# Performance work log

Measured on AMD Instinct MI355X. Metric: run time of the kernel, lower is better.

## Reference

```python
import jax, jax.numpy as jnp
import numpy as np

N, E, H, NF, EF = 50000, 1600000, 128, 8, 2


def setup_inputs() -> dict:
    key = jax.random.key(0)
    ks = jax.random.split(key, 24)
    rn = lambda k, shp, s=0.05: jax.random.normal(k, shp, jnp.float32) * s
    inp = {
        "x": jax.random.normal(ks[0], (N, NF), jnp.float32),
        "edge_index": jax.random.randint(ks[1], (2, E), 0, N),
        "edge_attr": jax.random.normal(ks[2], (E, EF), jnp.float32),
        "enc_W": rn(ks[3], (NF, H)),
        "enc_b": jnp.zeros((H,), jnp.float32),
        "bn_g": jnp.ones((H,), jnp.float32),
        "bn_b": jnp.zeros((H,), jnp.float32),
    }
    i = 4
    for l in (1, 2, 3):
        inp[f"W{l}"] = rn(ks[i], (H, H))
        inp[f"asrc{l}"] = rn(ks[i + 1], (H,))
        inp[f"adst{l}"] = rn(ks[i + 2], (H,))
        inp[f"We{l}"] = rn(ks[i + 3], (EF, H))
        inp[f"ae{l}"] = rn(ks[i + 4], (H,))
        inp[f"b{l}"] = jnp.zeros((H,), jnp.float32)
        i += 5
    return inp


def _gat(h, src, dst, ea, W, a_s, a_d, We, a_e, b, n):
    # PyG GATConv, heads=1, concat=True, negative_slope=0.2
    g = h @ W                                   # [N, H] transformed nodes
    a_src = g @ a_s                             # [N] per-source attention term
    a_dst = g @ a_d                             # [N] per-target attention term
    a_edge = (ea @ We) @ a_e                    # [E'] edge-conditioned term
    logit = jax.nn.leaky_relu(a_src[src] + a_dst[dst] + a_edge, negative_slope=0.2)
    # scatter-softmax over incoming edges of each destination node
    m = jax.ops.segment_max(logit, dst, num_segments=n)
    e = jnp.exp(logit - m[dst])
    s = jax.ops.segment_sum(e, dst, num_segments=n)
    alpha = e / (s[dst] + 1e-16)                # [E']
    out = jax.ops.segment_sum(g[src] * alpha[:, None], dst, num_segments=n)
    return out + b


def _forward(x, edge_index, edge_attr, enc_W, enc_b, bn_g, bn_b,
             W1, asrc1, adst1, We1, ae1, b1,
             W2, asrc2, adst2, We2, ae2, b2,
             W3, asrc3, adst3, We3, ae3, b3):
    n = x.shape[0]
    # PyG add_self_loops=True with fill_value='mean' for edge_attr
    loop = jnp.arange(n)
    src = jnp.concatenate([edge_index[0], loop])
    dst = jnp.concatenate([edge_index[1], loop])
    ea = jnp.concatenate([edge_attr, jnp.broadcast_to(edge_attr.mean(0), (n, edge_attr.shape[1]))], axis=0)
    # node encoder: Linear -> BatchNorm1d (eval: running_mean=0, running_var=1) -> ReLU (dropout off)
    inv = np.float32(1.0 / np.sqrt(1.0 + 1e-5))
    h0 = jax.nn.relu((x @ enc_W + enc_b) * (bn_g * inv) + bn_b)
    h1 = jax.nn.relu(_gat(h0, src, dst, ea, W1, asrc1, adst1, We1, ae1, b1, n))
    h2 = jax.nn.relu(_gat(h1, src, dst, ea, W2, asrc2, adst2, We2, ae2, b2, n))
    h3 = _gat(h2, src, dst, ea, W3, asrc3, adst3, We3, ae3, b3, n)
    return h3 + h0


def reference(x, edge_index, edge_attr, enc_W, enc_b, bn_g, bn_b,
              W1, asrc1, adst1, We1, ae1, b1,
              W2, asrc2, adst2, We2, ae2, b2,
              W3, asrc3, adst3, We3, ae3, b3):
    return _forward(x, edge_index, edge_attr, enc_W, enc_b, bn_g, bn_b,
                    W1, asrc1, adst1, We1, ae1, b1,
                    W2, asrc2, adst2, We2, ae2, b2,
                    W3, asrc3, adst3, We3, ae3, b3)
```

## Files before the change

### kernel.cpp

```cpp
#include <hip/hip_runtime.h>
#include <math.h>


#define H 128
#define NF 8
#define EPB 4096
#define GR 64

__device__ __forceinline__ float wred_sum(float x) {
#pragma unroll
    for (int m = 32; m >= 1; m >>= 1) x += __shfl_xor(x, m, 64);
    return x;
}
__device__ __forceinline__ float wred_max(float x) {
#pragma unroll
    for (int m = 32; m >= 1; m >>= 1) x = fmaxf(x, __shfl_xor(x, m, 64));
    return x;
}
__device__ __forceinline__ ushort f2bf(float f) {
    uint u = __float_as_uint(f);
    uint r = (u + 0x7FFFu + ((u >> 16) & 1u)) >> 16;
    return (ushort)r;
}


__global__ void k_count(const int* __restrict__ ei, const float* __restrict__ ea,
                        int E, int nblk, int nbuckets, int* __restrict__ bucketTotal,
                        int* __restrict__ blockBase, float2* __restrict__ pmean) {
    __shared__ int hist[256];
    __shared__ float sx[4], sy[4];
    int t = threadIdx.x;
    int blk = blockIdx.x;
    hist[t] = 0;
    __syncthreads();
    int base = blk * EPB;
    float px = 0.f, py = 0.f;
#pragma unroll
    for (int i = 0; i < 16; ++i) {
        int e = base + i * 256 + t;
        if (e < E) {
            int d = ei[E + e];
            atomicAdd(&hist[d >> 8], 1);
            const float2 z = *(const float2*)(ea + 2 * (size_t)e);
            px += z.x; py += z.y;
        }
    }
    px = wred_sum(px); py = wred_sum(py);
    if ((t & 63) == 0) { sx[t >> 6] = px; sy[t >> 6] = py; }
    __syncthreads();
    if (t == 0) {
        pmean[blk] = make_float2(sx[0] + sx[1] + sx[2] + sx[3],
                                 sy[0] + sy[1] + sy[2] + sy[3]);
    }
    if (t < nbuckets) {
        int c = hist[t];
        int old = (c > 0) ? atomicAdd(&bucketTotal[t], c) : 0;
        blockBase[t * nblk + blk] = old;
    }
}

__global__ void k_scan_park(const int* __restrict__ bucketTotal, int nbuckets,
                            int* __restrict__ bucketBase, int* __restrict__ rowptr,
                            int N, int E, const float2* __restrict__ pmean, int nblk,
                            float invE,
                            const float* __restrict__ We1, const float* __restrict__ ae1,
                            const float* __restrict__ We2, const float* __restrict__ ae2,
                            const float* __restrict__ We3, const float* __restrict__ ae3,
                            float* __restrict__ park) {
    __shared__ int tmp[256];
    __shared__ float2 sp[4];
    __shared__ float smean[2];
    int t = threadIdx.x;
    float ax = 0.f, ay = 0.f;
    for (int i = t; i < nblk; i += 256) {
        float2 z = pmean[i];
        ax += z.x; ay += z.y;
    }
    ax = wred_sum(ax); ay = wred_sum(ay);
    if ((t & 63) == 0) sp[t >> 6] = make_float2(ax, ay);
    int v = (t < nbuckets) ? bucketTotal[t] : 0;
    tmp[t] = v;
    __syncthreads();
    for (int off = 1; off < 256; off <<= 1) {
        int q = (t >= off) ? tmp[t - off] : 0;
        __syncthreads();
        tmp[t] += q;
        __syncthreads();
    }
    bucketBase[t] = tmp[t] - v;
    if (t == 0) {
        bucketBase[256] = tmp[255];
        rowptr[N] = E;
        smean[0] = (sp[0].x + sp[1].x + sp[2].x + sp[3].x) * invE;
        smean[1] = (sp[0].y + sp[1].y + sp[2].y + sp[3].y) * invE;
    }
    __syncthreads();
    if (t < 192) {
        int l = t >> 6, q = t & 63;
        const float* We = (l == 0) ? We1 : ((l == 1) ? We2 : We3);
        const float* ae = (l == 0) ? ae1 : ((l == 1) ? ae2 : ae3);
        float p0 = We[q] * ae[q] + We[q + 64] * ae[q + 64];
        float p1 = We[H + q] * ae[q] + We[H + q + 64] * ae[q + 64];
        p0 = wred_sum(p0);
        p1 = wred_sum(p1);
        if (q == 0) {
            park[l * 3 + 0] = p0;
            park[l * 3 + 1] = p1;
            park[l * 3 + 2] = smean[0] * p0 + smean[1] * p1;
        }
    }
}

__global__ void k_place(const int* __restrict__ ei, const float* __restrict__ ea,
                        int E, int nblk, int nbuckets,
                        const int* __restrict__ bucketBase, const int* __restrict__ blockBase,
                        uint2* __restrict__ temp) {
    __shared__ int cnt[256];
    __shared__ int sbase[256];
    int t = threadIdx.x;
    int blk = blockIdx.x;
    cnt[t] = 0;
    if (t < nbuckets) sbase[t] = bucketBase[t] + blockBase[t * nblk + blk];
    __syncthreads();
    int base = blk * EPB;
#pragma unroll
    for (int i = 0; i < 16; ++i) {
        int e = base + i * 256 + t;
        if (e < E) {
            int s = ei[e];
            int d = ei[E + e];
            int b = d >> 8;
            int r = atomicAdd(&cnt[b], 1);
            const float2 z = *(const float2*)(ea + 2 * (size_t)e);
            uint w0 = (uint)s | ((uint)(d & 255) << 16);
            uint w1 = (uint)f2bf(z.x) | ((uint)f2bf(z.y) << 16);
            temp[sbase[b] + r] = make_uint2(w0, w1);
        }
    }
}

__global__ void k_fine(const uint2* __restrict__ temp, const int* __restrict__ bucketBase,
                       const float* __restrict__ park, int N,
                       int4* __restrict__ erec, int* __restrict__ rowptr) {
    __shared__ int hist[256];
    __shared__ int tmp[256];
    __shared__ int fb[256];
    __shared__ int cur[256];
    int b = blockIdx.x;
    int t = threadIdx.x;
    const int lo = bucketBase[b], hi = bucketBase[b + 1];
    hist[t] = 0;
    __syncthreads();
    for (int e = lo + t; e < hi; e += 256) {
        atomicAdd(&hist[(temp[e].x >> 16) & 255], 1);
    }
    __syncthreads();
    int v = hist[t];
    tmp[t] = v;
    __syncthreads();
    for (int off = 1; off < 256; off <<= 1) {
        int q = (t >= off) ? tmp[t - off] : 0;
        __syncthreads();
        tmp[t] += q;
        __syncthreads();
    }
    fb[t] = tmp[t] - v;
    cur[t] = 0;
    int dst = b * 256 + t;
    if (dst < N) rowptr[dst] = lo + fb[t];
    __syncthreads();
    const float c00 = park[0], c01 = park[1];
    const float c10 = park[3], c11 = park[4];
    const float c20 = park[6], c21 = park[7];
    for (int e = lo + t; e < hi; e += 256) {
        uint2 w = temp[e];
        int src = (int)(w.x & 0xFFFFu);
        int j = (int)((w.x >> 16) & 255u);
        float ex = __uint_as_float(w.y << 16);
        float ey = __uint_as_float(w.y & 0xffff0000u);
        int r = atomicAdd(&cur[j], 1);
        float f0 = c00 * ex + c01 * ey;
        float f1 = c10 * ex + c11 * ey;
        float f2 = c20 * ex + c21 * ey;
        erec[lo + fb[j] + r] = make_int4(src, __float_as_int(f0),
                                         __float_as_int(f1), __float_as_int(f2));
    }
}

__global__ void k_encoder(const float* __restrict__ x, const float* __restrict__ encW,
                          const float* __restrict__ encb, const float* __restrict__ bng,
                          const float* __restrict__ bnb, float* __restrict__ h0, int N) {
    __shared__ float xs[8 * NF];
    int tid = threadIdx.x;
    int nb = blockIdx.x * 8;
    if (tid < 64) {
        size_t idx = (size_t)nb * NF + tid;
        xs[tid] = (idx < (size_t)N * NF) ? x[idx] : 0.f;
    }
    __syncthreads();
    int jt = tid & 31, i = tid >> 5;
    int node = nb + i;
    int j4 = jt * 4;
    float ax = 0.f, ay = 0.f, az = 0.f, aw = 0.f;
#pragma unroll
    for (int k = 0; k < NF; ++k) {
        float hx = xs[i * NF + k];
        const float4 w = *(const float4*)(encW + k * H + j4);
        ax = fmaf(hx, w.x, ax); ay = fmaf(hx, w.y, ay);
        az = fmaf(hx, w.z, az); aw = fmaf(hx, w.w, aw);
    }
    if (node < N) {
        const float inv = 0.9999950000374997f;
        const float4 eb = *(const float4*)(encb + j4);
        const float4 gg = *(const float4*)(bng + j4);
        const float4 bb = *(const float4*)(bnb + j4);
        float4 o;
        o.x = fmaxf(0.f, (ax + eb.x) * (gg.x * inv) + bb.x);
        o.y = fmaxf(0.f, (ay + eb.y) * (gg.y * inv) + bb.y);
        o.z = fmaxf(0.f, (az + eb.z) * (gg.z * inv) + bb.z);
        o.w = fmaxf(0.f, (aw + eb.w) * (gg.w * inv) + bb.w);
        *(float4*)(h0 + (size_t)node * H + j4) = o;
    }
}

__global__ void k_gemm(const float* __restrict__ h, const float* __restrict__ W,
                       const float* __restrict__ avs, const float* __restrict__ avd,
                       ushort* __restrict__ gb, float* __restrict__ a_src,
                       float* __restrict__ a_dst, int N) {
    __shared__ float hs[GR * H];
    int tid = threadIdx.x;
    int nb = blockIdx.x * GR;
#pragma unroll
    for (int it = 0; it < 8; ++it) {
        int fi = it * 256 + tid;
        int r = fi >> 5;
        int c4 = (fi & 31) * 4;
        int node = nb + r;
        float4 v = make_float4(0.f, 0.f, 0.f, 0.f);
        if (node < N) v = *(const float4*)(h + (size_t)node * H + c4);
        *(float4*)(hs + r * H + c4) = v;
    }
    __syncthreads();
    const int jt = tid & 31;
    const int ig = tid >> 5;
    const int j4 = jt * 4;
    const int r0 = ig * 8;

    float acc[8][4];
#pragma unroll
    for (int r = 0; r < 8; ++r)
#pragma unroll
        for (int c = 0; c < 4; ++c) acc[r][c] = 0.f;

    for (int k = 0; k < H; k += 4) {
        const float4 w0 = *(const float4*)(W + (k + 0) * H + j4);
        const float4 w1 = *(const float4*)(W + (k + 1) * H + j4);
        const float4 w2 = *(const float4*)(W + (k + 2) * H + j4);
        const float4 w3 = *(const float4*)(W + (k + 3) * H + j4);
#pragma unroll
        for (int r = 0; r < 8; ++r) {
            const float4 hv = *(const float4*)(hs + (r0 + r) * H + k);
            acc[r][0] = fmaf(hv.x, w0.x, acc[r][0]);
            acc[r][1] = fmaf(hv.x, w0.y, acc[r][1]);
            acc[r][2] = fmaf(hv.x, w0.z, acc[r][2]);
            acc[r][3] = fmaf(hv.x, w0.w, acc[r][3]);
            acc[r][0] = fmaf(hv.y, w1.x, acc[r][0]);
            acc[r][1] = fmaf(hv.y, w1.y, acc[r][1]);
            acc[r][2] = fmaf(hv.y, w1.z, acc[r][2]);
            acc[r][3] = fmaf(hv.y, w1.w, acc[r][3]);
            acc[r][0] = fmaf(hv.z, w2.x, acc[r][0]);
            acc[r][1] = fmaf(hv.z, w2.y, acc[r][1]);
            acc[r][2] = fmaf(hv.z, w2.z, acc[r][2]);
            acc[r][3] = fmaf(hv.z, w2.w, acc[r][3]);
            acc[r][0] = fmaf(hv.w, w3.x, acc[r][0]);
            acc[r][1] = fmaf(hv.w, w3.y, acc[r][1]);
            acc[r][2] = fmaf(hv.w, w3.z, acc[r][2]);
            acc[r][3] = fmaf(hv.w, w3.w, acc[r][3]);
        }
    }

    const float4 s4 = *(const float4*)(avs + j4);
    const float4 d4 = *(const float4*)(avd + j4);
#pragma unroll
    for (int r = 0; r < 8; ++r) {
        int node = nb + r0 + r;
        float ps = acc[r][0] * s4.x + acc[r][1] * s4.y + acc[r][2] * s4.z + acc[r][3] * s4.w;
        float pd = acc[r][0] * d4.x + acc[r][1] * d4.y + acc[r][2] * d4.z + acc[r][3] * d4.w;
#pragma unroll
        for (int mm = 16; mm >= 1; mm >>= 1) {
            ps += __shfl_xor(ps, mm, 64);
            pd += __shfl_xor(pd, mm, 64);
        }
        if (node < N) {
            ushort4 o;
            o.x = f2bf(acc[r][0]); o.y = f2bf(acc[r][1]);
            o.z = f2bf(acc[r][2]); o.w = f2bf(acc[r][3]);
            *(ushort4*)(gb + (size_t)node * H + j4) = o;
            if (jt == 0) {
                a_src[node] = ps;
                a_dst[node] = pd;
            }
        }
    }
}

template <int RELU, int ADDH0, int LAYER>
__global__ void k_agg(const ushort* __restrict__ gb, const float* __restrict__ a_src,
                      const float* __restrict__ a_dst, const int* __restrict__ rowptr,
                      const int4* __restrict__ erec, const float* __restrict__ park,
                      const float* __restrict__ bias, const float* __restrict__ h0,
                      float* __restrict__ out, int N) {
    int wv = threadIdx.x >> 6;
    int lane = threadIdx.x & 63;
    int v = blockIdx.x * 4 + wv;
    if (v >= N) return;

    const int grp = lane >> 4;
    const int sub = lane & 15;
    const int ch8 = sub * 8;

    const float sa = park[LAYER * 3 + 2];
    const float adv = a_dst[v];
    float lself = a_src[v] + adv + sa;
    lself = (lself > 0.f) ? lself : 0.2f * lself;

    float m = lself;
    float s = 1.f;
    float acc[8];
    {
        const uint4 q = *(const uint4*)(gb + (size_t)v * H + ch8);
        float sel = (grp == 0) ? 1.f : 0.f;
        acc[0] = sel * __uint_as_float(q.x << 16);
        acc[1] = sel * __uint_as_float(q.x & 0xffff0000u);
        acc[2] = sel * __uint_as_float(q.y << 16);
        acc[3] = sel * __uint_as_float(q.y & 0xffff0000u);
        acc[4] = sel * __uint_as_float(q.z << 16);
        acc[5] = sel * __uint_as_float(q.z & 0xffff0000u);
        acc[6] = sel * __uint_as_float(q.w << 16);
        acc[7] = sel * __uint_as_float(q.w & 0xffff0000u);
    }

    const int rs = rowptr[v];
    const int re = rowptr[v + 1];
    for (int p0 = rs; p0 < re; p0 += 64) {
        int e = p0 + lane;
        bool val = e < re;
        int4 rec = val ? erec[e] : make_int4(0, 0, 0, 0);
        int sv = rec.x;
        float lg;
        if (val) {
            float aef = __int_as_float(LAYER == 0 ? rec.y : (LAYER == 1 ? rec.z : rec.w));
            lg = a_src[sv] + adv + aef;
            lg = (lg > 0.f) ? lg : 0.2f * lg;
        } else {
            lg = -INFINITY;
        }
        float cm = wred_max(lg);
        float nm = fmaxf(m, cm);
        float f = __expf(m - nm);
        float w = val ? __expf(lg - nm) : 0.f;
        float ws = wred_sum(w);
        s = s * f + ws;
#pragma unroll
        for (int k = 0; k < 8; ++k) acc[k] *= f;
        m = nm;

        int cnt = re - p0;
        if (cnt > 64) cnt = 64;
        const int cm1 = cnt - 1;
        const int iters = (cnt + 7) >> 3;

        int jA = grp, jB = grp + 4;
        int jAc = (jA <= cm1) ? jA : cm1;
        int jBc = (jB <= cm1) ? jB : cm1;
        float wA = __shfl(w, jAc, 64); if (jA > cm1) wA = 0.f;
        float wB = __shfl(w, jBc, 64); if (jB > cm1) wB = 0.f;
        int sA = __shfl(sv, jAc, 64);
        int sB = __shfl(sv, jBc, 64);
        uint4 qA = *(const uint4*)(gb + (size_t)sA * H + ch8);
        uint4 qB = *(const uint4*)(gb + (size_t)sB * H + ch8);

        for (int i = 0; i < iters; ++i) {
            int jA1 = (i + 1) * 8 + grp, jB1 = jA1 + 4;
            int jA1c = (jA1 <= cm1) ? jA1 : cm1;
            int jB1c = (jB1 <= cm1) ? jB1 : cm1;
            float wA1 = __shfl(w, jA1c, 64); if (jA1 > cm1) wA1 = 0.f;
            float wB1 = __shfl(w, jB1c, 64); if (jB1 > cm1) wB1 = 0.f;
            int sA1 = __shfl(sv, jA1c, 64);
            int sB1 = __shfl(sv, jB1c, 64);
            uint4 qA1 = *(const uint4*)(gb + (size_t)sA1 * H + ch8);
            uint4 qB1 = *(const uint4*)(gb + (size_t)sB1 * H + ch8);

            acc[0] = fmaf(wA, __uint_as_float(qA.x << 16), acc[0]);
            acc[1] = fmaf(wA, __uint_as_float(qA.x & 0xffff0000u), acc[1]);
            acc[2] = fmaf(wA, __uint_as_float(qA.y << 16), acc[2]);
            acc[3] = fmaf(wA, __uint_as_float(qA.y & 0xffff0000u), acc[3]);
            acc[4] = fmaf(wA, __uint_as_float(qA.z << 16), acc[4]);
            acc[5] = fmaf(wA, __uint_as_float(qA.z & 0xffff0000u), acc[5]);
            acc[6] = fmaf(wA, __uint_as_float(qA.w << 16), acc[6]);
            acc[7] = fmaf(wA, __uint_as_float(qA.w & 0xffff0000u), acc[7]);
            acc[0] = fmaf(wB, __uint_as_float(qB.x << 16), acc[0]);
            acc[1] = fmaf(wB, __uint_as_float(qB.x & 0xffff0000u), acc[1]);
            acc[2] = fmaf(wB, __uint_as_float(qB.y << 16), acc[2]);
            acc[3] = fmaf(wB, __uint_as_float(qB.y & 0xffff0000u), acc[3]);
            acc[4] = fmaf(wB, __uint_as_float(qB.z << 16), acc[4]);
            acc[5] = fmaf(wB, __uint_as_float(qB.z & 0xffff0000u), acc[5]);
            acc[6] = fmaf(wB, __uint_as_float(qB.w << 16), acc[6]);
            acc[7] = fmaf(wB, __uint_as_float(qB.w & 0xffff0000u), acc[7]);

            wA = wA1; wB = wB1; qA = qA1; qB = qB1;
        }
    }

#pragma unroll
    for (int k = 0; k < 8; ++k) {
        acc[k] += __shfl_xor(acc[k], 16, 64);
        acc[k] += __shfl_xor(acc[k], 32, 64);
    }

    if (grp == 0) {
        const float is = 1.f / s;
        const float4 b0 = *(const float4*)(bias + ch8);
        const float4 b1 = *(const float4*)(bias + ch8 + 4);
        float o[8];
        o[0] = acc[0] * is + b0.x; o[1] = acc[1] * is + b0.y;
        o[2] = acc[2] * is + b0.z; o[3] = acc[3] * is + b0.w;
        o[4] = acc[4] * is + b1.x; o[5] = acc[5] * is + b1.y;
        o[6] = acc[6] * is + b1.z; o[7] = acc[7] * is + b1.w;
        if (ADDH0) {
            const float4 ha = *(const float4*)(h0 + (size_t)v * H + ch8);
            const float4 hb = *(const float4*)(h0 + (size_t)v * H + ch8 + 4);
            o[0] += ha.x; o[1] += ha.y; o[2] += ha.z; o[3] += ha.w;
            o[4] += hb.x; o[5] += hb.y; o[6] += hb.z; o[7] += hb.w;
        }
        if (RELU) {
#pragma unroll
            for (int k = 0; k < 8; ++k) o[k] = fmaxf(o[k], 0.f);
        }
        *(float4*)(out + (size_t)v * H + ch8) = make_float4(o[0], o[1], o[2], o[3]);
        *(float4*)(out + (size_t)v * H + ch8 + 4) = make_float4(o[4], o[5], o[6], o[7]);
    }
}


extern "C" void kernel_launch(void* const* d_in, const int* in_sizes, int n_in,
                              void* d_out, int out_size, void* d_ws, size_t ws_size,
                              hipStream_t stream) {
    const float* x    = (const float*)d_in[0];
    const int*   ei   = (const int*)d_in[1];
    const float* ea   = (const float*)d_in[2];
    const float* encW = (const float*)d_in[3];
    const float* encb = (const float*)d_in[4];
    const float* bng  = (const float*)d_in[5];
    const float* bnb  = (const float*)d_in[6];
    const float *W[3], *asrc[3], *adst[3], *We[3], *aev[3], *bias[3];
    for (int l = 0; l < 3; ++l) {
        W[l]    = (const float*)d_in[7 + l * 6 + 0];
        asrc[l] = (const float*)d_in[7 + l * 6 + 1];
        adst[l] = (const float*)d_in[7 + l * 6 + 2];
        We[l]   = (const float*)d_in[7 + l * 6 + 3];
        aev[l]  = (const float*)d_in[7 + l * 6 + 4];
        bias[l] = (const float*)d_in[7 + l * 6 + 5];
    }
    const int N = in_sizes[0] / NF;
    const int E = in_sizes[1] / 2;
    float* out = (float*)d_out;

    const int NBu  = (N + 255) >> 8;
    const int nblk = (E + EPB - 1) / EPB;

    char* wp = (char*)d_ws;
    auto alloc = [&](size_t bytes) -> char* {
        char* p = wp;
        wp += (bytes + 255) & ~(size_t)255;
        return p;
    };
    float*  h0       = (float*)alloc((size_t)N * H * 4);
    float*  hA       = (float*)alloc((size_t)N * H * 4);
    ushort* gb       = (ushort*)alloc((size_t)N * H * 2);
    float*  a_src    = (float*)alloc((size_t)N * 4);
    float*  a_dst    = (float*)alloc((size_t)N * 4);
    int*    rowptr   = (int*)alloc((size_t)(N + 1) * 4);
    float*  park     = (float*)alloc(64);
    int*    bucketTotal = (int*)alloc(256 * 4);
    int*    bucketBase  = (int*)alloc(257 * 4);
    int*    blockBase   = (int*)alloc((size_t)NBu * nblk * 4);
    int4*   erec     = (int4*)alloc((size_t)E * 16);
    float2* pmean    = (float2*)alloc((size_t)nblk * 8);
    uint2*  temp     = (uint2*)hA;

    hipMemsetAsync(bucketTotal, 0, 256 * 4, stream);

    k_count<<<nblk, 256, 0, stream>>>(ei, ea, E, nblk, NBu, bucketTotal, blockBase, pmean);
    k_scan_park<<<1, 256, 0, stream>>>(bucketTotal, NBu, bucketBase, rowptr, N, E,
                                       pmean, nblk, 1.0f / (float)E,
                                       We[0], aev[0], We[1], aev[1], We[2], aev[2], park);
    k_place<<<nblk, 256, 0, stream>>>(ei, ea, E, nblk, NBu, bucketBase, blockBase, temp);
    k_fine<<<NBu, 256, 0, stream>>>(temp, bucketBase, park, N, erec, rowptr);

    const int GB8 = (N + 7) / 8;
    const int GBR = (N + GR - 1) / GR;
    const int AB = (N + 3) / 4;
    k_encoder<<<GB8, 256, 0, stream>>>(x, encW, encb, bng, bnb, h0, N);

    k_gemm<<<GBR, 256, 0, stream>>>(h0, W[0], asrc[0], adst[0], gb, a_src, a_dst, N);
    k_agg<1, 0, 0><<<AB, 256, 0, stream>>>(gb, a_src, a_dst, rowptr, erec, park,
                                           bias[0], nullptr, hA, N);
    k_gemm<<<GBR, 256, 0, stream>>>(hA, W[1], asrc[1], adst[1], gb, a_src, a_dst, N);
    k_agg<1, 0, 1><<<AB, 256, 0, stream>>>(gb, a_src, a_dst, rowptr, erec, park,
                                           bias[1], nullptr, hA, N);
    k_gemm<<<GBR, 256, 0, stream>>>(hA, W[2], asrc[2], adst[2], gb, a_src, a_dst, N);
    k_agg<0, 1, 2><<<AB, 256, 0, stream>>>(gb, a_src, a_dst, rowptr, erec, park,
                                           bias[2], h0, out, N);
}
```

Measured before the change: 356.4 us.

## Use bf16 MFMA for node GEMMs, bf16 hidden states, compact per-layer edge records

Replaces the fp32 FMA GEMM with a bf16 MFMA 16x16x32 kernel fed by prepacked weights and bf16 node features, which the encoder and aggregation kernels now emit. Edge records shrink from a 16-byte int4 holding all layers to one 4-byte word per layer, packing the 16-bit source index with the bf16 edge logit term. This cuts GEMM compute time and memory traffic in both the GEMM and the edge gather. The cost is lower precision in the hidden states and edge terms. The 16-bit source packing only holds while N stays at or below 65536.

```diff
diff --git a/kernel.cpp b/kernel.cpp
--- a/kernel.cpp
+++ b/kernel.cpp
@@ -5,7 +5,9 @@
 #define H 128
 #define NF 8
 #define EPB 4096
-#define GR 64
+
+typedef __attribute__((ext_vector_type(8))) short short8v;
+typedef __attribute__((ext_vector_type(4))) float f32x4;
 
 __device__ __forceinline__ float wred_sum(float x) {
 #pragma unroll
@@ -141,7 +143,8 @@
 
 __global__ void k_fine(const uint2* __restrict__ temp, const int* __restrict__ bucketBase,
                        const float* __restrict__ park, int N,
-                       int4* __restrict__ erec, int* __restrict__ rowptr) {
+                       uint* __restrict__ er0, uint* __restrict__ er1,
+                       uint* __restrict__ er2, int* __restrict__ rowptr) {
     __shared__ int hist[256];
     __shared__ int tmp[256];
     __shared__ int fb[256];
@@ -174,22 +177,37 @@
     const float c20 = park[6], c21 = park[7];
     for (int e = lo + t; e < hi; e += 256) {
         uint2 w = temp[e];
-        int src = (int)(w.x & 0xFFFFu);
+        uint src = w.x & 0xFFFFu;
         int j = (int)((w.x >> 16) & 255u);
         float ex = __uint_as_float(w.y << 16);
         float ey = __uint_as_float(w.y & 0xffff0000u);
         int r = atomicAdd(&cur[j], 1);
-        float f0 = c00 * ex + c01 * ey;
-        float f1 = c10 * ex + c11 * ey;
-        float f2 = c20 * ex + c21 * ey;
-        erec[lo + fb[j] + r] = make_int4(src, __float_as_int(f0),
-                                         __float_as_int(f1), __float_as_int(f2));
+        int p = lo + fb[j] + r;
+        er0[p] = src | ((uint)f2bf(c00 * ex + c01 * ey) << 16);
+        er1[p] = src | ((uint)f2bf(c10 * ex + c11 * ey) << 16);
+        er2[p] = src | ((uint)f2bf(c20 * ex + c21 * ey) << 16);
+    }
+}
+
+__global__ void k_wpack(const float* __restrict__ W1, const float* __restrict__ W2,
+                        const float* __restrict__ W3, ushort* __restrict__ Wp) {
+    int layer = blockIdx.x;
+    const float* W = (layer == 0) ? W1 : ((layer == 1) ? W2 : W3);
+    for (int idx = threadIdx.x; idx < 16384; idx += 256) {
+        int i = idx & 7;
+        int lane = (idx >> 3) & 63;
+        int ft = idx >> 9;
+        int kt = ft & 3, nt = ft >> 2;
+        int k = kt * 32 + (lane >> 4) * 8 + i;
+        int n = nt * 16 + (lane & 15);
+        Wp[layer * 16384 + idx] = f2bf(W[k * H + n]);
     }
 }
 
 __global__ void k_encoder(const float* __restrict__ x, const float* __restrict__ encW,
                           const float* __restrict__ encb, const float* __restrict__ bng,
-                          const float* __restrict__ bnb, float* __restrict__ h0, int N) {
+                          const float* __restrict__ bnb, float* __restrict__ h0,
+                          ushort* __restrict__ hb, int N) {
     __shared__ float xs[8 * NF];
     int tid = threadIdx.x;
     int nb = blockIdx.x * 8;
@@ -220,96 +238,95 @@
         o.z = fmaxf(0.f, (az + eb.z) * (gg.z * inv) + bb.z);
         o.w = fmaxf(0.f, (aw + eb.w) * (gg.w * inv) + bb.w);
         *(float4*)(h0 + (size_t)node * H + j4) = o;
-    }
-}
-
-__global__ void k_gemm(const float* __restrict__ h, const float* __restrict__ W,
-                       const float* __restrict__ avs, const float* __restrict__ avd,
-                       ushort* __restrict__ gb, float* __restrict__ a_src,
-                       float* __restrict__ a_dst, int N) {
-    __shared__ float hs[GR * H];
+        uint2 ob;
+        ob.x = (uint)f2bf(o.x) | ((uint)f2bf(o.y) << 16);
+        ob.y = (uint)f2bf(o.z) | ((uint)f2bf(o.w) << 16);
+        *(uint2*)(hb + (size_t)node * H + j4) = ob;
+    }
+}
+
+__global__ void k_gemm_mfma(const ushort* __restrict__ hb, const ushort* __restrict__ Wp,
+                            const float* __restrict__ avs, const float* __restrict__ avd,
+                            ushort* __restrict__ gb, float* __restrict__ a_src,
+                            float* __restrict__ a_dst, int N) {
+    __shared__ ushort hs[64 * 136];
     int tid = threadIdx.x;
-    int nb = blockIdx.x * GR;
-#pragma unroll
-    for (int it = 0; it < 8; ++it) {
+    int nb = blockIdx.x * 64;
+#pragma unroll
+    for (int it = 0; it < 4; ++it) {
         int fi = it * 256 + tid;
-        int r = fi >> 5;
-        int c4 = (fi & 31) * 4;
+        int r = fi >> 4;
+        int c8 = (fi & 15) * 8;
         int node = nb + r;
-        float4 v = make_float4(0.f, 0.f, 0.f, 0.f);
-        if (node < N) v = *(const float4*)(h + (size_t)node * H + c4);
-        *(float4*)(hs + r * H + c4) = v;
-    }
-    __syncthreads();
-    const int jt = tid & 31;
-    const int ig = tid >> 5;
-    const int j4 = jt * 4;
-    const int r0 = ig * 8;
-
-    float acc[8][4];
-#pragma unroll
-    for (int r = 0; r < 8; ++r)
-#pragma unroll
-        for (int c = 0; c < 4; ++c) acc[r][c] = 0.f;
-
-    for (int k = 0; k < H; k += 4) {
-        const float4 w0 = *(const float4*)(W + (k + 0) * H + j4);
-        const float4 w1 = *(const float4*)(W + (k + 1) * H + j4);
-        const float4 w2 = *(const float4*)(W + (k + 2) * H + j4);
-        const float4 w3 = *(const float4*)(W + (k + 3) * H + j4);
-#pragma unroll
-        for (int r = 0; r < 8; ++r) {
-            const float4 hv = *(const float4*)(hs + (r0 + r) * H + k);
-            acc[r][0] = fmaf(hv.x, w0.x, acc[r][0]);
-            acc[r][1] = fmaf(hv.x, w0.y, acc[r][1]);
-            acc[r][2] = fmaf(hv.x, w0.z, acc[r][2]);
-            acc[r][3] = fmaf(hv.x, w0.w, acc[r][3]);
-            acc[r][0] = fmaf(hv.y, w1.x, acc[r][0]);
-            acc[r][1] = fmaf(hv.y, w1.y, acc[r][1]);
-            acc[r][2] = fmaf(hv.y, w1.z, acc[r][2]);
-            acc[r][3] = fmaf(hv.y, w1.w, acc[r][3]);
-            acc[r][0] = fmaf(hv.z, w2.x, acc[r][0]);
-            acc[r][1] = fmaf(hv.z, w2.y, acc[r][1]);
-            acc[r][2] = fmaf(hv.z, w2.z, acc[r][2]);
-            acc[r][3] = fmaf(hv.z, w2.w, acc[r][3]);
-            acc[r][0] = fmaf(hv.w, w3.x, acc[r][0]);
-            acc[r][1] = fmaf(hv.w, w3.y, acc[r][1]);
-            acc[r][2] = fmaf(hv.w, w3.z, acc[r][2]);
-            acc[r][3] = fmaf(hv.w, w3.w, acc[r][3]);
-        }
-    }
-
-    const float4 s4 = *(const float4*)(avs + j4);
-    const float4 d4 = *(const float4*)(avd + j4);
-#pragma unroll
-    for (int r = 0; r < 8; ++r) {
-        int node = nb + r0 + r;
-        float ps = acc[r][0] * s4.x + acc[r][1] * s4.y + acc[r][2] * s4.z + acc[r][3] * s4.w;
-        float pd = acc[r][0] * d4.x + acc[r][1] * d4.y + acc[r][2] * d4.z + acc[r][3] * d4.w;
-#pragma unroll
-        for (int mm = 16; mm >= 1; mm >>= 1) {
-            ps += __shfl_xor(ps, mm, 64);
-            pd += __shfl_xor(pd, mm, 64);
-        }
-        if (node < N) {
-            ushort4 o;
-            o.x = f2bf(acc[r][0]); o.y = f2bf(acc[r][1]);
-            o.z = f2bf(acc[r][2]); o.w = f2bf(acc[r][3]);
-            *(ushort4*)(gb + (size_t)node * H + j4) = o;
-            if (jt == 0) {
-                a_src[node] = ps;
-                a_dst[node] = pd;
-            }
-        }
-    }
-}
-
-template <int RELU, int ADDH0, int LAYER>
+        uint4 v = make_uint4(0, 0, 0, 0);
+        if (node < N) v = *(const uint4*)(hb + (size_t)node * H + c8);
+        *(uint4*)(hs + r * 136 + c8) = v;
+    }
+    __syncthreads();
+    const int l = tid & 63;
+    const int w = tid >> 6;
+    const int cl = l & 15;
+    const int kg = l >> 4;
+    const ushort* hrow = hs + (w * 16 + cl) * 136 + kg * 8;
+    short8v a0 = *(const short8v*)(hrow + 0);
+    short8v a1 = *(const short8v*)(hrow + 32);
+    short8v a2 = *(const short8v*)(hrow + 64);
+    short8v a3 = *(const short8v*)(hrow + 96);
+
+    f32x4 acc[8];
+#pragma unroll
+    for (int nt = 0; nt < 8; ++nt) {
+        const short8v* bp = (const short8v*)(Wp + ((size_t)(nt * 4) * 64 + l) * 8);
+        f32x4 c = {0.f, 0.f, 0.f, 0.f};
+        c = __builtin_amdgcn_mfma_f32_16x16x32_bf16(a0, bp[0], c, 0, 0, 0);
+        c = __builtin_amdgcn_mfma_f32_16x16x32_bf16(a1, bp[64], c, 0, 0, 0);
+        c = __builtin_amdgcn_mfma_f32_16x16x32_bf16(a2, bp[128], c, 0, 0, 0);
+        c = __builtin_amdgcn_mfma_f32_16x16x32_bf16(a3, bp[192], c, 0, 0, 0);
+        acc[nt] = c;
+    }
+
+    float ps0 = 0.f, ps1 = 0.f, ps2 = 0.f, ps3 = 0.f;
+    float pd0 = 0.f, pd1 = 0.f, pd2 = 0.f, pd3 = 0.f;
+#pragma unroll
+    for (int nt = 0; nt < 8; ++nt) {
+        float vs = avs[cl + 16 * nt];
+        float vd = avd[cl + 16 * nt];
+        ps0 = fmaf(acc[nt].x, vs, ps0); pd0 = fmaf(acc[nt].x, vd, pd0);
+        ps1 = fmaf(acc[nt].y, vs, ps1); pd1 = fmaf(acc[nt].y, vd, pd1);
+        ps2 = fmaf(acc[nt].z, vs, ps2); pd2 = fmaf(acc[nt].z, vd, pd2);
+        ps3 = fmaf(acc[nt].w, vs, ps3); pd3 = fmaf(acc[nt].w, vd, pd3);
+    }
+#pragma unroll
+    for (int m = 8; m >= 1; m >>= 1) {
+        ps0 += __shfl_xor(ps0, m, 64); pd0 += __shfl_xor(pd0, m, 64);
+        ps1 += __shfl_xor(ps1, m, 64); pd1 += __shfl_xor(pd1, m, 64);
+        ps2 += __shfl_xor(ps2, m, 64); pd2 += __shfl_xor(pd2, m, 64);
+        ps3 += __shfl_xor(ps3, m, 64); pd3 += __shfl_xor(pd3, m, 64);
+    }
+    int r0 = nb + w * 16 + kg * 4;
+    if (cl == 0) {
+        if (r0 + 0 < N) { a_src[r0 + 0] = ps0; a_dst[r0 + 0] = pd0; }
+        if (r0 + 1 < N) { a_src[r0 + 1] = ps1; a_dst[r0 + 1] = pd1; }
+        if (r0 + 2 < N) { a_src[r0 + 2] = ps2; a_dst[r0 + 2] = pd2; }
+        if (r0 + 3 < N) { a_src[r0 + 3] = ps3; a_dst[r0 + 3] = pd3; }
+    }
+#pragma unroll
+    for (int nt = 0; nt < 8; ++nt) {
+        int col = nt * 16 + cl;
+        if (r0 + 0 < N) gb[(size_t)(r0 + 0) * H + col] = f2bf(acc[nt].x);
+        if (r0 + 1 < N) gb[(size_t)(r0 + 1) * H + col] = f2bf(acc[nt].y);
+        if (r0 + 2 < N) gb[(size_t)(r0 + 2) * H + col] = f2bf(acc[nt].z);
+        if (r0 + 3 < N) gb[(size_t)(r0 + 3) * H + col] = f2bf(acc[nt].w);
+    }
+}
+
+template <int MODE>
 __global__ void k_agg(const ushort* __restrict__ gb, const float* __restrict__ a_src,
                       const float* __restrict__ a_dst, const int* __restrict__ rowptr,
-                      const int4* __restrict__ erec, const float* __restrict__ park,
-                      const float* __restrict__ bias, const float* __restrict__ h0,
-                      float* __restrict__ out, int N) {
+                      const uint* __restrict__ erecL, const float* __restrict__ park,
+                      int layer, const float* __restrict__ bias,
+                      const float* __restrict__ h0, float* __restrict__ outf,
+                      ushort* __restrict__ outb, int N) {
     int wv = threadIdx.x >> 6;
     int lane = threadIdx.x & 63;
     int v = blockIdx.x * 4 + wv;
@@ -319,7 +336,7 @@
     const int sub = lane & 15;
     const int ch8 = sub * 8;
 
-    const float sa = park[LAYER * 3 + 2];
+    const float sa = park[layer * 3 + 2];
     const float adv = a_dst[v];
     float lself = a_src[v] + adv + sa;
     lself = (lself > 0.f) ? lself : 0.2f * lself;
@@ -345,11 +362,11 @@
     for (int p0 = rs; p0 < re; p0 += 64) {
         int e = p0 + lane;
         bool val = e < re;
-        int4 rec = val ? erec[e] : make_int4(0, 0, 0, 0);
-        int sv = rec.x;
+        uint rec = val ? erecL[e] : 0u;
+        int sv = (int)(rec & 0xFFFFu);
         float lg;
         if (val) {
-            float aef = __int_as_float(LAYER == 0 ? rec.y : (LAYER == 1 ? rec.z : rec.w));
+            float aef = __uint_as_float(rec & 0xffff0000u);
             lg = a_src[sv] + adv + aef;
             lg = (lg > 0.f) ? lg : 0.2f * lg;
         } else {
@@ -427,18 +444,23 @@
         o[2] = acc[2] * is + b0.z; o[3] = acc[3] * is + b0.w;
         o[4] = acc[4] * is + b1.x; o[5] = acc[5] * is + b1.y;
         o[6] = acc[6] * is + b1.z; o[7] = acc[7] * is + b1.w;
-        if (ADDH0) {
+        if (MODE == 0) {
+#pragma unroll
+            for (int k = 0; k < 8; ++k) o[k] = fmaxf(o[k], 0.f);
+            uint4 ob;
+            ob.x = (uint)f2bf(o[0]) | ((uint)f2bf(o[1]) << 16);
+            ob.y = (uint)f2bf(o[2]) | ((uint)f2bf(o[3]) << 16);
+            ob.z = (uint)f2bf(o[4]) | ((uint)f2bf(o[5]) << 16);
+            ob.w = (uint)f2bf(o[6]) | ((uint)f2bf(o[7]) << 16);
+            *(uint4*)(outb + (size_t)v * H + ch8) = ob;
+        } else {
             const float4 ha = *(const float4*)(h0 + (size_t)v * H + ch8);
-            const float4 hb = *(const float4*)(h0 + (size_t)v * H + ch8 + 4);
+            const float4 hb4 = *(const float4*)(h0 + (size_t)v * H + ch8 + 4);
             o[0] += ha.x; o[1] += ha.y; o[2] += ha.z; o[3] += ha.w;
-            o[4] += hb.x; o[5] += hb.y; o[6] += hb.z; o[7] += hb.w;
+            o[4] += hb4.x; o[5] += hb4.y; o[6] += hb4.z; o[7] += hb4.w;
+            *(float4*)(outf + (size_t)v * H + ch8) = make_float4(o[0], o[1], o[2], o[3]);
+            *(float4*)(outf + (size_t)v * H + ch8 + 4) = make_float4(o[4], o[5], o[6], o[7]);
         }
-        if (RELU) {
-#pragma unroll
-            for (int k = 0; k < 8; ++k) o[k] = fmaxf(o[k], 0.f);
-        }
-        *(float4*)(out + (size_t)v * H + ch8) = make_float4(o[0], o[1], o[2], o[3]);
-        *(float4*)(out + (size_t)v * H + ch8 + 4) = make_float4(o[4], o[5], o[6], o[7]);
     }
 }
 
@@ -476,8 +498,9 @@
         return p;
     };
     float*  h0       = (float*)alloc((size_t)N * H * 4);
-    float*  hA       = (float*)alloc((size_t)N * H * 4);
+    ushort* hb       = (ushort*)alloc((size_t)N * H * 2);
     ushort* gb       = (ushort*)alloc((size_t)N * H * 2);
+    ushort* Wp       = (ushort*)alloc((size_t)3 * 16384 * 2);
     float*  a_src    = (float*)alloc((size_t)N * 4);
     float*  a_dst    = (float*)alloc((size_t)N * 4);
     int*    rowptr   = (int*)alloc((size_t)(N + 1) * 4);
@@ -485,9 +508,11 @@
     int*    bucketTotal = (int*)alloc(256 * 4);
     int*    bucketBase  = (int*)alloc(257 * 4);
     int*    blockBase   = (int*)alloc((size_t)NBu * nblk * 4);
-    int4*   erec     = (int4*)alloc((size_t)E * 16);
+    uint*   er0      = (uint*)alloc((size_t)E * 4);
+    uint*   er1      = (uint*)alloc((size_t)E * 4);
+    uint*   er2      = (uint*)alloc((size_t)E * 4);
     float2* pmean    = (float2*)alloc((size_t)nblk * 8);
-    uint2*  temp     = (uint2*)hA;
+    uint2*  temp     = (uint2*)h0;
 
     hipMemsetAsync(bucketTotal, 0, 256 * 4, stream);
 
@@ -496,20 +521,24 @@
                                        pmean, nblk, 1.0f / (float)E,
                                        We[0], aev[0], We[1], aev[1], We[2], aev[2], park);
     k_place<<<nblk, 256, 0, stream>>>(ei, ea, E, nblk, NBu, bucketBase, blockBase, temp);
-    k_fine<<<NBu, 256, 0, stream>>>(temp, bucketBase, park, N, erec, rowptr);
+    k_fine<<<NBu, 256, 0, stream>>>(temp, bucketBase, park, N, er0, er1, er2, rowptr);
+    k_wpack<<<3, 256, 0, stream>>>(W[0], W[1], W[2], Wp);
 
     const int GB8 = (N + 7) / 8;
-    const int GBR = (N + GR - 1) / GR;
+    const int GBM = (N + 63) / 64;
     const int AB = (N + 3) / 4;
-    k_encoder<<<GB8, 256, 0, stream>>>(x, encW, encb, bng, bnb, h0, N);
-
-    k_gemm<<<GBR, 256, 0, stream>>>(h0, W[0], asrc[0], adst[0], gb, a_src, a_dst, N);
-    k_agg<1, 0, 0><<<AB, 256, 0, stream>>>(gb, a_src, a_dst, rowptr, erec, park,
-                                           bias[0], nullptr, hA, N);
-    k_gemm<<<GBR, 256, 0, stream>>>(hA, W[1], asrc[1], adst[1], gb, a_src, a_dst, N);
-    k_agg<1, 0, 1><<<AB, 256, 0, stream>>>(gb, a_src, a_dst, rowptr, erec, park,
-                                           bias[1], nullptr, hA, N);
-    k_gemm<<<GBR, 256, 0, stream>>>(hA, W[2], asrc[2], adst[2], gb, a_src, a_dst, N);
-    k_agg<0, 1, 2><<<AB, 256, 0, stream>>>(gb, a_src, a_dst, rowptr, erec, park,
-                                           bias[2], h0, out, N);
-}
+    k_encoder<<<GB8, 256, 0, stream>>>(x, encW, encb, bng, bnb, h0, hb, N);
+
+    k_gemm_mfma<<<GBM, 256, 0, stream>>>(hb, Wp + 0 * 16384, asrc[0], adst[0],
+                                         gb, a_src, a_dst, N);
+    k_agg<0><<<AB, 256, 0, stream>>>(gb, a_src, a_dst, rowptr, er0, park, 0,
+                                     bias[0], nullptr, nullptr, hb, N);
+    k_gemm_mfma<<<GBM, 256, 0, stream>>>(hb, Wp + 1 * 16384, asrc[1], adst[1],
+                                         gb, a_src, a_dst, N);
+    k_agg<0><<<AB, 256, 0, stream>>>(gb, a_src, a_dst, rowptr, er1, park, 1,
+                                     bias[1], nullptr, nullptr, hb, N);
+    k_gemm_mfma<<<GBM, 256, 0, stream>>>(hb, Wp + 2 * 16384, asrc[2], adst[2],
+                                         gb, a_src, a_dst, N);
+    k_agg<1><<<AB, 256, 0, stream>>>(gb, a_src, a_dst, rowptr, er2, park, 2,
+                                     bias[2], h0, out, nullptr, N);
+}
```

Measured after the change: 313.1 us. -12.2%, faster.
